# Kernel tuning notes

Hardware: AMD Instinct MI355X
Metric: run time of the kernel (lower is better)

Reference implementation:

```python
import jax, jax.numpy as jnp
import numpy as np

N = 100000      # nodes
E = 1600000     # edges (before self loops)
F_IN = 256      # num_features
HID = 8         # hid per head, layer 1
H1 = 8          # in_head
H2 = 4          # out_head
NCLS = 40       # num_classes


def setup_inputs() -> dict:
    key = jax.random.key(0)
    ks = jax.random.split(key, 10)
    p = lambda k, shape: jax.random.normal(k, shape, jnp.float32) * 0.1
    d1 = H1 * HID   # 64
    d2 = H2 * NCLS  # 160
    return dict(
        x=jax.random.normal(ks[0], (N, F_IN), jnp.float32),
        edge_index=jax.random.randint(ks[1], (2, E), 0, N),
        Wl1=p(ks[2], (F_IN, d1)), bl1=jnp.zeros((d1,), jnp.float32),
        Wr1=p(ks[3], (F_IN, d1)), br1=jnp.zeros((d1,), jnp.float32),
        att1=p(ks[4], (H1, HID)), b1=jnp.zeros((d1,), jnp.float32),
        Wl2=p(ks[5], (d1, d2)), bl2=jnp.zeros((d2,), jnp.float32),
        Wr2=p(ks[6], (d1, d2)), br2=jnp.zeros((d2,), jnp.float32),
        att2=p(ks[7], (H2, NCLS)), b2=jnp.zeros((NCLS,), jnp.float32),
    )


def gatv2_conv(x, src, dst, Wl, bl, Wr, br, att, bias, heads, ch, concat):
    """PyG GATv2Conv (eval mode): lin_l -> source/messages, lin_r -> target."""
    n = x.shape[0]
    xl = (x @ Wl + bl).reshape(n, heads, ch)   # source-side features
    xr = (x @ Wr + br).reshape(n, heads, ch)   # target-side features
    # edge-wise attention logits: LeakyReLU(x_i + x_j) . att
    e = jax.nn.leaky_relu(xl[src] + xr[dst], 0.2)          # [E, H, C]
    logits = jnp.einsum('ehc,hc->eh', e, att)               # [E, H]
    # segment softmax over incoming edges of each destination node
    m = jax.ops.segment_max(logits, dst, num_segments=n)    # [N, H]
    ex = jnp.exp(logits - m[dst])
    s = jax.ops.segment_sum(ex, dst, num_segments=n)        # [N, H]
    alpha = ex / (s[dst] + 1e-16)                           # [E, H]
    # scatter-add weighted source messages
    out = jax.ops.segment_sum(xl[src] * alpha[:, :, None], dst, num_segments=n)  # [N, H, C]
    if concat:
        return out.reshape(n, heads * ch) + bias
    return out.mean(axis=1) + bias


def reference(x, edge_index, Wl1, bl1, Wr1, br1, att1, b1,
              Wl2, bl2, Wr2, br2, att2, b2):
    n = x.shape[0]
    loop = jnp.arange(n)
    # PyG GATv2Conv default add_self_loops=True
    src = jnp.concatenate([edge_index[0], loop])
    dst = jnp.concatenate([edge_index[1], loop])
    # eval mode: all dropout (input, inter-layer, attention) disabled
    h = gatv2_conv(x, src, dst, Wl1, bl1, Wr1, br1, att1, b1, H1, HID, True)
    h = jax.nn.elu(h)
    out = gatv2_conv(h, src, dst, Wl2, bl2, Wr2, br2, att2, b2, H2, NCLS, False)
    return jax.nn.log_softmax(out, axis=1)
```

## Files before the change

kernel.cpp:

```cpp
#include <hip/hip_runtime.h>
#include <math.h>

#define NN 100000
#define EE 1600000
#define FIN 256
#define D1 64
#define D2 160
#define C2 40
#define P1R 72
#define P2R 168
#define PK1 264
#define PK2 72
#define NBUCK 391
#define CAP 5000

typedef unsigned short u16;
typedef __attribute__((ext_vector_type(8))) short bf16x8;
typedef __attribute__((ext_vector_type(4))) float f32x4;

__device__ __forceinline__ float bf2f(u16 u){ return __uint_as_float((unsigned)u << 16); }
__device__ __forceinline__ u16 f2bf(float f){
  unsigned b = __float_as_uint(f);
  return (u16)((b + 0x7FFFu + ((b >> 16) & 1u)) >> 16);
}

__global__ void wprep_k(const float* __restrict__ Wl1, const float* __restrict__ Wr1,
                        const float* __restrict__ att1,
                        const float* __restrict__ bl1, const float* __restrict__ br1,
                        const float* __restrict__ Wl2, const float* __restrict__ Wr2,
                        const float* __restrict__ att2,
                        const float* __restrict__ bl2, const float* __restrict__ br2,
                        float* __restrict__ WA1, float* __restrict__ BA1,
                        float* __restrict__ WA2, float* __restrict__ BA2){
  int t = blockIdx.x*256 + threadIdx.x;
  if (t < 4096){
    int k = t >> 4, j = t & 15;
    float v = 0.f;
    if (j < 8){
      float s = 0.f;
      #pragma unroll
      for (int c = 0; c < 8; ++c) s += Wl1[(size_t)k*D1 + j*8 + c] * att1[j*8 + c];
      v = 0.6f * s;
    }
    WA1[t] = v;
  } else if (t < 4608){
    int i = t - 4096;
    int k = i >> 3, j = i & 7;
    float v = 0.f;
    if (j < 4){
      float s = 0.f;
      #pragma unroll
      for (int c = 0; c < 40; ++c) s += Wl2[(size_t)k*D2 + j*40 + c] * att2[j*40 + c];
      v = 0.6f * s;
    }
    WA2[i] = v;
  } else if (t < 4616){
    int j = t - 4608;
    float s = 0.f;
    #pragma unroll
    for (int c = 0; c < 8; ++c) s += bl1[j*8 + c] * att1[j*8 + c];
    BA1[j] = 0.6f * s;
  } else if (t < 4620){
    int j = t - 4616;
    float s = 0.f;
    #pragma unroll
    for (int c = 0; c < 40; ++c) s += bl2[j*40 + c] * att2[j*40 + c];
    BA2[j] = 0.6f * s;
  }
}

__global__ __launch_bounds__(256) void part1_k(const int* __restrict__ ei,
                                               int* __restrict__ bcnt,
                                               int* __restrict__ csrtmp){
  __shared__ int hist[NBUCK];
  __shared__ int gbase[NBUCK];
  int t = threadIdx.x;
  for (int i = t; i < NBUCK; i += 256) hist[i] = 0;
  __syncthreads();
  int rb[8], rr[8], rv[8];
  #pragma unroll
  for (int q = 0; q < 8; ++q){
    int e = blockIdx.x*2048 + q*256 + t;
    rb[q] = -1;
    if (e < EE){
      int s = ei[e], d = ei[EE + e];
      int b = d >> 8;
      rb[q] = b;
      rv[q] = s | ((d & 255) << 17);
      rr[q] = atomicAdd(&hist[b], 1);
    }
  }
  __syncthreads();
  for (int i = t; i < NBUCK; i += 256)
    if (hist[i] > 0) gbase[i] = atomicAdd(&bcnt[i], hist[i]);
  __syncthreads();
  #pragma unroll
  for (int q = 0; q < 8; ++q){
    if (rb[q] >= 0){
      int pos = gbase[rb[q]] + rr[q];
      if (pos < CAP) csrtmp[rb[q]*CAP + pos] = rv[q];
    }
  }
}

__global__ __launch_bounds__(256) void sort_k(const int* __restrict__ bcnt,
                                              const int* __restrict__ csrtmp,
                                              int* __restrict__ csr,
                                              int* __restrict__ off,
                                              int* __restrict__ end){
  __shared__ int cnt[256];
  __shared__ int sc[256];
  __shared__ int cur[256];
  int b = blockIdx.x, t = threadIdx.x;
  int E = bcnt[b]; if (E > CAP) E = CAP;
  int n = (b << 8) + t;
  cnt[t] = (n < NN) ? 1 : 0;
  __syncthreads();
  for (int i = t; i < E; i += 256){
    int v = csrtmp[b*CAP + i];
    atomicAdd(&cnt[(v >> 17) & 255], 1);
  }
  __syncthreads();
  int x = cnt[t];
  sc[t] = x;
  __syncthreads();
  for (int o = 1; o < 256; o <<= 1){
    int v = (t >= o) ? sc[t - o] : 0;
    __syncthreads();
    sc[t] += v;
    __syncthreads();
  }
  int excl = sc[t] - x;
  if (n < NN){
    off[n] = b*CAP + excl;
    end[n] = b*CAP + excl + x;
    csr[b*CAP + excl] = n;
    cur[t] = excl + 1;
  } else {
    cur[t] = excl;
  }
  __syncthreads();
  for (int i = t; i < E; i += 256){
    int v = csrtmp[b*CAP + i];
    int p = atomicAdd(&cur[(v >> 17) & 255], 1);
    csr[b*CAP + p] = v & 0x1FFFF;
  }
}

__global__ __launch_bounds__(256) void gemm1_mfma(
    const float* __restrict__ X,
    const float* __restrict__ Wl, const float* __restrict__ bl,
    const float* __restrict__ Wr, const float* __restrict__ br,
    const float* __restrict__ WA1, const float* __restrict__ BA1,
    u16* __restrict__ outl, u16* __restrict__ outr){
  __shared__ u16 WB[144*PK1];
  int t = threadIdx.x;
  #pragma unroll
  for (int q = 0; q < 16; ++q){
    int idx = t + 256*q;
    int k = idx >> 4, c4 = idx & 15;
    float4 vl = *reinterpret_cast<const float4*>(Wl + (size_t)k*D1 + c4*4);
    float4 vr = *reinterpret_cast<const float4*>(Wr + (size_t)k*D1 + c4*4);
    WB[(c4*4+0)*PK1 + k] = f2bf(vl.x); WB[(c4*4+1)*PK1 + k] = f2bf(vl.y);
    WB[(c4*4+2)*PK1 + k] = f2bf(vl.z); WB[(c4*4+3)*PK1 + k] = f2bf(vl.w);
    WB[(64+c4*4+0)*PK1 + k] = f2bf(vr.x); WB[(64+c4*4+1)*PK1 + k] = f2bf(vr.y);
    WB[(64+c4*4+2)*PK1 + k] = f2bf(vr.z); WB[(64+c4*4+3)*PK1 + k] = f2bf(vr.w);
  }
  #pragma unroll
  for (int q = 0; q < 16; ++q){
    int idx = t + 256*q;
    int k = idx >> 4, j = idx & 15;
    WB[(128+j)*PK1 + k] = f2bf(WA1[k*16 + j]);
  }
  __syncthreads();
  int w = t >> 6, l = t & 63;
  int g = l >> 4;
  int arow = blockIdx.x*64 + w*16 + (l & 15);
  if (arow >= NN) arow = NN-1;
  const float* xp = X + (size_t)arow*FIN + g*8;
  f32x4 acc[9] = {};
  #pragma unroll
  for (int kk = 0; kk < 8; ++kk){
    float4 a0 = *reinterpret_cast<const float4*>(xp + kk*32);
    float4 a1 = *reinterpret_cast<const float4*>(xp + kk*32 + 4);
    union { bf16x8 v; u16 u[8]; } A;
    A.u[0]=f2bf(a0.x); A.u[1]=f2bf(a0.y); A.u[2]=f2bf(a0.z); A.u[3]=f2bf(a0.w);
    A.u[4]=f2bf(a1.x); A.u[5]=f2bf(a1.y); A.u[6]=f2bf(a1.z); A.u[7]=f2bf(a1.w);
    const u16* wb = WB + (l & 15)*PK1 + kk*32 + g*8;
    #pragma unroll
    for (int c = 0; c < 9; ++c){
      bf16x8 B = *reinterpret_cast<const bf16x8*>(wb + c*16*PK1);
      acc[c] = __builtin_amdgcn_mfma_f32_16x16x32_bf16(A.v, B, acc[c], 0, 0, 0);
    }
  }
  int ocol = l & 15;
  int orow0 = blockIdx.x*64 + w*16 + g*4;
  #pragma unroll
  for (int c = 0; c < 8; ++c){
    bool left = (c < 4);
    int col = (left ? c : c-4)*16 + ocol;
    u16* op = left ? outl : outr;
    float bv = (left ? bl : br)[col];
    #pragma unroll
    for (int r = 0; r < 4; ++r){
      int row = orow0 + r;
      if (row < NN) op[(size_t)row*P1R + col] = f2bf(acc[c][r] + bv);
    }
  }
  if (ocol < 8){
    float bav = BA1[ocol];
    #pragma unroll
    for (int r = 0; r < 4; ++r){
      int row = orow0 + r;
      if (row < NN) outl[(size_t)row*P1R + 64 + ocol] = f2bf(__expf(acc[8][r] + bav));
    }
  }
}

__global__ __launch_bounds__(256) void gemm2_mfma(
    const u16* __restrict__ H,
    const float* __restrict__ Wl, const float* __restrict__ bl,
    const float* __restrict__ Wr, const float* __restrict__ br,
    const float* __restrict__ WA2, const float* __restrict__ BA2,
    u16* __restrict__ outl, u16* __restrict__ outr){
  __shared__ u16 WB[336*PK2];
  int t = threadIdx.x;
  #pragma unroll
  for (int q = 0; q < 10; ++q){
    int idx = t + 256*q;
    int k = idx / 40, c4 = idx % 40;
    float4 vl = *reinterpret_cast<const float4*>(Wl + (size_t)k*D2 + c4*4);
    float4 vr = *reinterpret_cast<const float4*>(Wr + (size_t)k*D2 + c4*4);
    WB[(c4*4+0)*PK2 + k] = f2bf(vl.x); WB[(c4*4+1)*PK2 + k] = f2bf(vl.y);
    WB[(c4*4+2)*PK2 + k] = f2bf(vl.z); WB[(c4*4+3)*PK2 + k] = f2bf(vl.w);
    WB[(160+c4*4+0)*PK2 + k] = f2bf(vr.x); WB[(160+c4*4+1)*PK2 + k] = f2bf(vr.y);
    WB[(160+c4*4+2)*PK2 + k] = f2bf(vr.z); WB[(160+c4*4+3)*PK2 + k] = f2bf(vr.w);
  }
  #pragma unroll
  for (int q = 0; q < 2; ++q){
    int i2 = t + 256*q;
    int k = i2 >> 3, j = i2 & 7;
    WB[(320+j)*PK2 + k] = f2bf(WA2[k*8 + j]);
    WB[(328+j)*PK2 + k] = 0;
  }
  __syncthreads();
  int w = t >> 6, l = t & 63;
  int g = l >> 4;
  int arow = blockIdx.x*64 + w*16 + (l & 15);
  if (arow >= NN) arow = NN-1;
  const u16* hp = H + (size_t)arow*D1 + g*8;
  f32x4 acc[21] = {};
  #pragma unroll
  for (int kk = 0; kk < 2; ++kk){
    bf16x8 A = *reinterpret_cast<const bf16x8*>(hp + kk*32);
    const u16* wb = WB + (l & 15)*PK2 + kk*32 + g*8;
    #pragma unroll
    for (int c = 0; c < 21; ++c){
      bf16x8 B = *reinterpret_cast<const bf16x8*>(wb + c*16*PK2);
      acc[c] = __builtin_amdgcn_mfma_f32_16x16x32_bf16(A, B, acc[c], 0, 0, 0);
    }
  }
  int ocol = l & 15;
  int orow0 = blockIdx.x*64 + w*16 + g*4;
  #pragma unroll
  for (int c = 0; c < 20; ++c){
    bool left = (c < 10);
    int col = (left ? c : c-10)*16 + ocol;
    u16* op = left ? outl : outr;
    float bv = (left ? bl : br)[col];
    #pragma unroll
    for (int r = 0; r < 4; ++r){
      int row = orow0 + r;
      if (row < NN) op[(size_t)row*P2R + col] = f2bf(acc[c][r] + bv);
    }
  }
  if (ocol < 4){
    float bav = BA2[ocol];
    #pragma unroll
    for (int r = 0; r < 4; ++r){
      int row = orow0 + r;
      if (row < NN) outl[(size_t)row*P2R + 160 + ocol] = f2bf(__expf(acc[20][r] + bav));
    }
  }
}

__global__ void l1_fused(const u16* __restrict__ xl, const u16* __restrict__ xr,
                         const int* __restrict__ off, const int* __restrict__ end,
                         const int* __restrict__ csr,
                         const float* __restrict__ att,
                         const float* __restrict__ b, u16* __restrict__ out){
  int tid = threadIdx.x;
  int lane = tid & 63;
  int g = (lane >> 4) & 1, l = lane & 15;
  int n = blockIdx.x*8 + (tid >> 6)*2 + (lane >> 5);
  if (n >= NN) return;
  int h = l >> 1;
  ushort4 xru = *reinterpret_cast<const ushort4*>(xr + (size_t)n*P1R + 4*l);
  float xrv[4] = {bf2f(xru.x), bf2f(xru.y), bf2f(xru.z), bf2f(xru.w)};
  float a04[4];
  #pragma unroll
  for (int k = 0; k < 4; ++k) a04[k] = 0.4f * att[4*l + k];
  float s = 0.f, acc[4] = {};
  int p = off[n] + g, e1 = end[n];
  for (; p + 6 < e1; p += 8){
    int sv[4];
    #pragma unroll
    for (int q = 0; q < 4; ++q) sv[q] = csr[p + 2*q];
    ushort4 uv[4]; float wv[4];
    #pragma unroll
    for (int q = 0; q < 4; ++q){
      uv[q] = *reinterpret_cast<const ushort4*>(xl + (size_t)sv[q]*P1R + 4*l);
      wv[q] = bf2f(xl[(size_t)sv[q]*P1R + 64 + h]);
    }
    #pragma unroll
    for (int q = 0; q < 4; ++q){
      float xa[4] = {bf2f(uv[q].x), bf2f(uv[q].y), bf2f(uv[q].z), bf2f(uv[q].w)};
      float ta = 0.f;
      #pragma unroll
      for (int k = 0; k < 4; ++k) ta = fmaf(a04[k], fabsf(xa[k] + xrv[k]), ta);
      ta += __shfl_xor(ta, 1);
      float pa = __expf(ta) * wv[q];
      s += pa;
      #pragma unroll
      for (int k = 0; k < 4; ++k) acc[k] = fmaf(pa, xa[k], acc[k]);
    }
  }
  for (; p < e1; p += 2){
    int sa = csr[p];
    ushort4 ua = *reinterpret_cast<const ushort4*>(xl + (size_t)sa*P1R + 4*l);
    float wA = bf2f(xl[(size_t)sa*P1R + 64 + h]);
    float xa[4] = {bf2f(ua.x), bf2f(ua.y), bf2f(ua.z), bf2f(ua.w)};
    float ta = 0.f;
    #pragma unroll
    for (int k = 0; k < 4; ++k) ta = fmaf(a04[k], fabsf(xa[k] + xrv[k]), ta);
    ta += __shfl_xor(ta, 1);
    float pa = __expf(ta) * wA;
    s += pa;
    #pragma unroll
    for (int k = 0; k < 4; ++k) acc[k] = fmaf(pa, xa[k], acc[k]);
  }
  s += __shfl_xor(s, 16);
  #pragma unroll
  for (int k = 0; k < 4; ++k) acc[k] += __shfl_xor(acc[k], 16);
  if (g == 0){
    float inv = 1.f / (s + 1e-16f);
    ushort4 o;
    float v0 = acc[0]*inv + b[4*l+0]; o.x = f2bf(v0 > 0.f ? v0 : expm1f(v0));
    float v1 = acc[1]*inv + b[4*l+1]; o.y = f2bf(v1 > 0.f ? v1 : expm1f(v1));
    float v2 = acc[2]*inv + b[4*l+2]; o.z = f2bf(v2 > 0.f ? v2 : expm1f(v2));
    float v3 = acc[3]*inv + b[4*l+3]; o.w = f2bf(v3 > 0.f ? v3 : expm1f(v3));
    *reinterpret_cast<ushort4*>(out + (size_t)n*D1 + 4*l) = o;
  }
}

__global__ void l2_fused(const u16* __restrict__ xl, const u16* __restrict__ xr,
                         const int* __restrict__ off, const int* __restrict__ end,
                         const int* __restrict__ csr,
                         const float* __restrict__ att,
                         const float* __restrict__ b, float* __restrict__ out){
  int tid = threadIdx.x;
  int lane = tid & 63;
  int g = (lane >> 4) & 1, l = lane & 15;
  int n = blockIdx.x*8 + (tid >> 6)*2 + (lane >> 5);
  if (n >= NN) return;
  int h = l >> 2;
  int c0 = 10*l;
  float xrv[10], a04[10];
  #pragma unroll
  for (int k2 = 0; k2 < 5; ++k2){
    ushort2 u = *reinterpret_cast<const ushort2*>(xr + (size_t)n*P2R + c0 + 2*k2);
    xrv[2*k2] = bf2f(u.x); xrv[2*k2+1] = bf2f(u.y);
  }
  #pragma unroll
  for (int k = 0; k < 10; ++k) a04[k] = 0.4f * att[c0 + k];
  float s = 0.f, acc[10] = {};
  int p = off[n] + g, e1 = end[n];
  for (; p + 2 < e1; p += 4){
    int sa = csr[p], sb = csr[p+2];
    const u16* ra = xl + (size_t)sa*P2R + c0;
    const u16* rb = xl + (size_t)sb*P2R + c0;
    int dwa[5], dwb[5];
    #pragma unroll
    for (int d = 0; d < 5; ++d) dwa[d] = *reinterpret_cast<const int*>(ra + 2*d);
    #pragma unroll
    for (int d = 0; d < 5; ++d) dwb[d] = *reinterpret_cast<const int*>(rb + 2*d);
    float wA = bf2f(xl[(size_t)sa*P2R + 160 + h]);
    float wB = bf2f(xl[(size_t)sb*P2R + 160 + h]);
    float xa[10], xb[10];
    #pragma unroll
    for (int d = 0; d < 5; ++d){
      xa[2*d]   = __uint_as_float(((unsigned)dwa[d]) << 16);
      xa[2*d+1] = __uint_as_float(((unsigned)dwa[d]) & 0xFFFF0000u);
      xb[2*d]   = __uint_as_float(((unsigned)dwb[d]) << 16);
      xb[2*d+1] = __uint_as_float(((unsigned)dwb[d]) & 0xFFFF0000u);
    }
    float ta = 0.f, tb = 0.f;
    #pragma unroll
    for (int k = 0; k < 10; ++k){
      ta = fmaf(a04[k], fabsf(xa[k] + xrv[k]), ta);
      tb = fmaf(a04[k], fabsf(xb[k] + xrv[k]), tb);
    }
    ta += __shfl_xor(ta, 1); ta += __shfl_xor(ta, 2);
    tb += __shfl_xor(tb, 1); tb += __shfl_xor(tb, 2);
    float pa = __expf(ta) * wA;
    float pb = __expf(tb) * wB;
    s += pa + pb;
    #pragma unroll
    for (int k = 0; k < 10; ++k) acc[k] = fmaf(pa, xa[k], fmaf(pb, xb[k], acc[k]));
  }
  for (; p < e1; p += 2){
    int sa = csr[p];
    const u16* rp = xl + (size_t)sa*P2R + c0;
    float wA = bf2f(xl[(size_t)sa*P2R + 160 + h]);
    float xa[10];
    #pragma unroll
    for (int d = 0; d < 5; ++d){
      int u = *reinterpret_cast<const int*>(rp + 2*d);
      xa[2*d]   = __uint_as_float(((unsigned)u) << 16);
      xa[2*d+1] = __uint_as_float(((unsigned)u) & 0xFFFF0000u);
    }
    float ta = 0.f;
    #pragma unroll
    for (int k = 0; k < 10; ++k) ta = fmaf(a04[k], fabsf(xa[k] + xrv[k]), ta);
    ta += __shfl_xor(ta, 1); ta += __shfl_xor(ta, 2);
    float pa = __expf(ta) * wA;
    s += pa;
    #pragma unroll
    for (int k = 0; k < 10; ++k) acc[k] = fmaf(pa, xa[k], acc[k]);
  }
  s += __shfl_xor(s, 16);
  #pragma unroll
  for (int k = 0; k < 10; ++k) acc[k] += __shfl_xor(acc[k], 16);
  float inv = 1.f / (s + 1e-16f);
  float v[10];
  #pragma unroll
  for (int k = 0; k < 10; ++k){
    float o = acc[k] * inv;
    o += __shfl_xor(o, 4);
    o += __shfl_xor(o, 8);
    v[k] = o*0.25f + b[10*(l & 3) + k];
  }
  float mx = v[0];
  #pragma unroll
  for (int k = 1; k < 10; ++k) mx = fmaxf(mx, v[k]);
  mx = fmaxf(mx, __shfl_xor(mx, 1));
  mx = fmaxf(mx, __shfl_xor(mx, 2));
  float es = 0.f;
  #pragma unroll
  for (int k = 0; k < 10; ++k) es += __expf(v[k] - mx);
  es += __shfl_xor(es, 1);
  es += __shfl_xor(es, 2);
  float lse = mx + __logf(es);
  if (g == 0 && l < 4){
    float* op = out + (size_t)n*C2 + 10*l;
    #pragma unroll
    for (int k2 = 0; k2 < 5; ++k2)
      *reinterpret_cast<float2*>(op + 2*k2) = make_float2(v[2*k2] - lse, v[2*k2+1] - lse);
  }
}

extern "C" void kernel_launch(void* const* d_in, const int* in_sizes, int n_in,
                              void* d_out, int out_size, void* d_ws, size_t ws_size,
                              hipStream_t stream){
  const float* x    = (const float*)d_in[0];
  const int*   ei   = (const int*)  d_in[1];
  const float* Wl1  = (const float*)d_in[2];
  const float* bl1  = (const float*)d_in[3];
  const float* Wr1  = (const float*)d_in[4];
  const float* br1  = (const float*)d_in[5];
  const float* att1 = (const float*)d_in[6];
  const float* b1   = (const float*)d_in[7];
  const float* Wl2  = (const float*)d_in[8];
  const float* bl2  = (const float*)d_in[9];
  const float* Wr2  = (const float*)d_in[10];
  const float* br2  = (const float*)d_in[11];
  const float* att2 = (const float*)d_in[12];
  const float* b2   = (const float*)d_in[13];
  float* out = (float*)d_out;

  char* ws = (char*)d_ws;
  u16*   B1     = (u16*)  (ws);
  u16*   B2     = (u16*)  (ws + 15000000);
  u16*   h1     = (u16*)  (ws + 30000000);
  u16*   B3     = (u16*)  (ws + 43000000);
  u16*   B4     = (u16*)  (ws + 77000000);
  int*   csrtmp = (int*)  (ws + 77000000);
  float* WA1    = (float*)(ws + 111000000);
  float* BA1    = (float*)(ws + 111100000);
  float* WA2    = (float*)(ws + 111200000);
  float* BA2    = (float*)(ws + 111300000);
  int*   off    = (int*)  (ws + 111400000);
  int*   end    = (int*)  (ws + 111900000);
  int*   bcnt   = (int*)  (ws + 112400000);
  int*   csr    = (int*)  (ws + 112500000);
  const int blk = 256;
  const int MB = (NN + 63)/64;

  hipMemsetAsync(bcnt, 0, (size_t)NBUCK*4, stream);
  part1_k<<<(EE + 2047)/2048, blk, 0, stream>>>(ei, bcnt, csrtmp);
  sort_k <<<NBUCK, blk, 0, stream>>>(bcnt, csrtmp, csr, off, end);
  wprep_k<<<19, blk, 0, stream>>>(Wl1, Wr1, att1, bl1, br1,
                                  Wl2, Wr2, att2, bl2, br2, WA1, BA1, WA2, BA2);

  gemm1_mfma<<<MB, blk, 0, stream>>>(x, Wl1, bl1, Wr1, br1, WA1, BA1, B1, B2);
  l1_fused  <<<(NN + 7)/8, blk, 0, stream>>>(B1, B2, off, end, csr, att1, b1, h1);

  gemm2_mfma<<<MB, blk, 0, stream>>>(h1, Wl2, bl2, Wr2, br2, WA2, BA2, B3, B4);
  l2_fused  <<<(NN + 7)/8, blk, 0, stream>>>(B3, B4, off, end, csr, att2, b2, out);
}
```

Before: 353.2 us.

## Switch GAT edge features to fp16 and use packed half2 math in aggregation

The GEMM epilogues now store the node features as fp16 instead of bf16, and the per-node attention weight is scaled by 1/64. The edge loops in both layers do the LeakyReLU-dot and the weighted accumulation with packed half2 FMAs rather than per-element fp32 math. The aim is to halve the ALU instruction count in the gather-bound aggregation kernels and drop the bf16 unpacking work. The risk is reduced precision and possible overflow in the fp16 accumulators, which the 1/64 scaling partly guards against, though some accuracy is lost.

```diff
diff --git a/kernel.cpp b/kernel.cpp
--- a/kernel.cpp
+++ b/kernel.cpp
@@ -13,15 +13,23 @@
 #define PK2 72
 #define NBUCK 391
 #define CAP 5000
+#define WSCL 0.015625f
 
 typedef unsigned short u16;
 typedef __attribute__((ext_vector_type(8))) short bf16x8;
 typedef __attribute__((ext_vector_type(4))) float f32x4;
-
-__device__ __forceinline__ float bf2f(u16 u){ return __uint_as_float((unsigned)u << 16); }
+typedef _Float16 h2t __attribute__((ext_vector_type(2)));
+union hu { unsigned u; h2t h; };
+
 __device__ __forceinline__ u16 f2bf(float f){
   unsigned b = __float_as_uint(f);
   return (u16)((b + 0x7FFFu + ((b >> 16) & 1u)) >> 16);
+}
+__device__ __forceinline__ u16 f2h(float f){
+  union { _Float16 h; u16 u; } c; c.h = (_Float16)f; return c.u;
+}
+__device__ __forceinline__ float h16f(u16 v){
+  union { u16 u; _Float16 h; } c; c.u = v; return (float)c.h;
 }
 
 __global__ void wprep_k(const float* __restrict__ Wl1, const float* __restrict__ Wr1,
@@ -204,7 +212,7 @@
     #pragma unroll
     for (int r = 0; r < 4; ++r){
       int row = orow0 + r;
-      if (row < NN) op[(size_t)row*P1R + col] = f2bf(acc[c][r] + bv);
+      if (row < NN) op[(size_t)row*P1R + col] = f2h(acc[c][r] + bv);
     }
   }
   if (ocol < 8){
@@ -212,7 +220,7 @@
     #pragma unroll
     for (int r = 0; r < 4; ++r){
       int row = orow0 + r;
-      if (row < NN) outl[(size_t)row*P1R + 64 + ocol] = f2bf(__expf(acc[8][r] + bav));
+      if (row < NN) outl[(size_t)row*P1R + 64 + ocol] = f2h(__expf(acc[8][r] + bav) * WSCL);
     }
   }
 }
@@ -271,7 +279,7 @@
     #pragma unroll
     for (int r = 0; r < 4; ++r){
       int row = orow0 + r;
-      if (row < NN) op[(size_t)row*P2R + col] = f2bf(acc[c][r] + bv);
+      if (row < NN) op[(size_t)row*P2R + col] = f2h(acc[c][r] + bv);
     }
   }
   if (ocol < 4){
@@ -279,7 +287,7 @@
     #pragma unroll
     for (int r = 0; r < 4; ++r){
       int row = orow0 + r;
-      if (row < NN) outl[(size_t)row*P2R + 160 + ocol] = f2bf(__expf(acc[20][r] + bav));
+      if (row < NN) outl[(size_t)row*P2R + 160 + ocol] = f2h(__expf(acc[20][r] + bav) * WSCL);
     }
   }
 }
@@ -295,60 +303,69 @@
   int n = blockIdx.x*8 + (tid >> 6)*2 + (lane >> 5);
   if (n >= NN) return;
   int h = l >> 1;
-  ushort4 xru = *reinterpret_cast<const ushort4*>(xr + (size_t)n*P1R + 4*l);
-  float xrv[4] = {bf2f(xru.x), bf2f(xru.y), bf2f(xru.z), bf2f(xru.w)};
-  float a04[4];
-  #pragma unroll
-  for (int k = 0; k < 4; ++k) a04[k] = 0.4f * att[4*l + k];
-  float s = 0.f, acc[4] = {};
+  uint2 xru = *reinterpret_cast<const uint2*>(xr + (size_t)n*P1R + 4*l);
+  hu r0, r1; r0.u = xru.x; r1.u = xru.y;
+  hu a0, a1;
+  a0.h[0] = (_Float16)(0.4f*att[4*l+0]); a0.h[1] = (_Float16)(0.4f*att[4*l+1]);
+  a1.h[0] = (_Float16)(0.4f*att[4*l+2]); a1.h[1] = (_Float16)(0.4f*att[4*l+3]);
+  float s = 0.f;
+  hu acc0, acc1; acc0.u = 0; acc1.u = 0;
   int p = off[n] + g, e1 = end[n];
   for (; p + 6 < e1; p += 8){
     int sv[4];
     #pragma unroll
     for (int q = 0; q < 4; ++q) sv[q] = csr[p + 2*q];
-    ushort4 uv[4]; float wv[4];
+    uint2 uv[4]; u16 wv[4];
     #pragma unroll
     for (int q = 0; q < 4; ++q){
-      uv[q] = *reinterpret_cast<const ushort4*>(xl + (size_t)sv[q]*P1R + 4*l);
-      wv[q] = bf2f(xl[(size_t)sv[q]*P1R + 64 + h]);
+      uv[q] = *reinterpret_cast<const uint2*>(xl + (size_t)sv[q]*P1R + 4*l);
+      wv[q] = xl[(size_t)sv[q]*P1R + 64 + h];
     }
     #pragma unroll
     for (int q = 0; q < 4; ++q){
-      float xa[4] = {bf2f(uv[q].x), bf2f(uv[q].y), bf2f(uv[q].z), bf2f(uv[q].w)};
-      float ta = 0.f;
-      #pragma unroll
-      for (int k = 0; k < 4; ++k) ta = fmaf(a04[k], fabsf(xa[k] + xrv[k]), ta);
-      ta += __shfl_xor(ta, 1);
-      float pa = __expf(ta) * wv[q];
+      hu x0, x1; x0.u = uv[q].x; x1.u = uv[q].y;
+      hu y0, y1; y0.h = x0.h + r0.h; y1.h = x1.h + r1.h;
+      y0.u &= 0x7FFF7FFFu; y1.u &= 0x7FFF7FFFu;
+      hu t2; t2.h = a0.h*y0.h + a1.h*y1.h;
+      float tf = (float)t2.h[0] + (float)t2.h[1];
+      tf += __shfl_xor(tf, 1);
+      float pa = __expf(tf) * h16f(wv[q]);
       s += pa;
-      #pragma unroll
-      for (int k = 0; k < 4; ++k) acc[k] = fmaf(pa, xa[k], acc[k]);
+      hu pp; pp.h[0] = (_Float16)pa; pp.h[1] = pp.h[0];
+      acc0.h = pp.h*x0.h + acc0.h;
+      acc1.h = pp.h*x1.h + acc1.h;
     }
   }
   for (; p < e1; p += 2){
     int sa = csr[p];
-    ushort4 ua = *reinterpret_cast<const ushort4*>(xl + (size_t)sa*P1R + 4*l);
-    float wA = bf2f(xl[(size_t)sa*P1R + 64 + h]);
-    float xa[4] = {bf2f(ua.x), bf2f(ua.y), bf2f(ua.z), bf2f(ua.w)};
-    float ta = 0.f;
-    #pragma unroll
-    for (int k = 0; k < 4; ++k) ta = fmaf(a04[k], fabsf(xa[k] + xrv[k]), ta);
-    ta += __shfl_xor(ta, 1);
-    float pa = __expf(ta) * wA;
+    uint2 ua = *reinterpret_cast<const uint2*>(xl + (size_t)sa*P1R + 4*l);
+    u16 wa = xl[(size_t)sa*P1R + 64 + h];
+    hu x0, x1; x0.u = ua.x; x1.u = ua.y;
+    hu y0, y1; y0.h = x0.h + r0.h; y1.h = x1.h + r1.h;
+    y0.u &= 0x7FFF7FFFu; y1.u &= 0x7FFF7FFFu;
+    hu t2; t2.h = a0.h*y0.h + a1.h*y1.h;
+    float tf = (float)t2.h[0] + (float)t2.h[1];
+    tf += __shfl_xor(tf, 1);
+    float pa = __expf(tf) * h16f(wa);
     s += pa;
-    #pragma unroll
-    for (int k = 0; k < 4; ++k) acc[k] = fmaf(pa, xa[k], acc[k]);
+    hu pp; pp.h[0] = (_Float16)pa; pp.h[1] = pp.h[0];
+    acc0.h = pp.h*x0.h + acc0.h;
+    acc1.h = pp.h*x1.h + acc1.h;
   }
   s += __shfl_xor(s, 16);
-  #pragma unroll
-  for (int k = 0; k < 4; ++k) acc[k] += __shfl_xor(acc[k], 16);
+  { hu m; m.u = (unsigned)__shfl_xor((int)acc0.u, 16); acc0.h = acc0.h + m.h; }
+  { hu m; m.u = (unsigned)__shfl_xor((int)acc1.u, 16); acc1.h = acc1.h + m.h; }
   if (g == 0){
     float inv = 1.f / (s + 1e-16f);
+    float v0 = (float)acc0.h[0]*inv + b[4*l+0];
+    float v1 = (float)acc0.h[1]*inv + b[4*l+1];
+    float v2 = (float)acc1.h[0]*inv + b[4*l+2];
+    float v3 = (float)acc1.h[1]*inv + b[4*l+3];
     ushort4 o;
-    float v0 = acc[0]*inv + b[4*l+0]; o.x = f2bf(v0 > 0.f ? v0 : expm1f(v0));
-    float v1 = acc[1]*inv + b[4*l+1]; o.y = f2bf(v1 > 0.f ? v1 : expm1f(v1));
-    float v2 = acc[2]*inv + b[4*l+2]; o.z = f2bf(v2 > 0.f ? v2 : expm1f(v2));
-    float v3 = acc[3]*inv + b[4*l+3]; o.w = f2bf(v3 > 0.f ? v3 : expm1f(v3));
+    o.x = f2bf(v0 > 0.f ? v0 : expm1f(v0));
+    o.y = f2bf(v1 > 0.f ? v1 : expm1f(v1));
+    o.z = f2bf(v2 > 0.f ? v2 : expm1f(v2));
+    o.w = f2bf(v3 > 0.f ? v3 : expm1f(v3));
     *reinterpret_cast<ushort4*>(out + (size_t)n*D1 + 4*l) = o;
   }
 }
@@ -365,77 +382,91 @@
   if (n >= NN) return;
   int h = l >> 2;
   int c0 = 10*l;
-  float xrv[10], a04[10];
-  #pragma unroll
-  for (int k2 = 0; k2 < 5; ++k2){
-    ushort2 u = *reinterpret_cast<const ushort2*>(xr + (size_t)n*P2R + c0 + 2*k2);
-    xrv[2*k2] = bf2f(u.x); xrv[2*k2+1] = bf2f(u.y);
-  }
-  #pragma unroll
-  for (int k = 0; k < 10; ++k) a04[k] = 0.4f * att[c0 + k];
-  float s = 0.f, acc[10] = {};
+  hu xr2[5], a2[5];
+  #pragma unroll
+  for (int d = 0; d < 5; ++d){
+    xr2[d].u = *reinterpret_cast<const unsigned*>(xr + (size_t)n*P2R + c0 + 2*d);
+    a2[d].h[0] = (_Float16)(0.4f*att[c0 + 2*d]);
+    a2[d].h[1] = (_Float16)(0.4f*att[c0 + 2*d + 1]);
+  }
+  float s = 0.f;
+  hu acc2[5];
+  #pragma unroll
+  for (int d = 0; d < 5; ++d) acc2[d].u = 0;
   int p = off[n] + g, e1 = end[n];
   for (; p + 2 < e1; p += 4){
     int sa = csr[p], sb = csr[p+2];
     const u16* ra = xl + (size_t)sa*P2R + c0;
     const u16* rb = xl + (size_t)sb*P2R + c0;
-    int dwa[5], dwb[5];
-    #pragma unroll
-    for (int d = 0; d < 5; ++d) dwa[d] = *reinterpret_cast<const int*>(ra + 2*d);
-    #pragma unroll
-    for (int d = 0; d < 5; ++d) dwb[d] = *reinterpret_cast<const int*>(rb + 2*d);
-    float wA = bf2f(xl[(size_t)sa*P2R + 160 + h]);
-    float wB = bf2f(xl[(size_t)sb*P2R + 160 + h]);
-    float xa[10], xb[10];
+    hu xa[5], xb[5];
+    #pragma unroll
+    for (int d = 0; d < 5; ++d) xa[d].u = *reinterpret_cast<const unsigned*>(ra + 2*d);
+    #pragma unroll
+    for (int d = 0; d < 5; ++d) xb[d].u = *reinterpret_cast<const unsigned*>(rb + 2*d);
+    u16 wa16 = xl[(size_t)sa*P2R + 160 + h];
+    u16 wb16 = xl[(size_t)sb*P2R + 160 + h];
+    hu ta2, tb2; ta2.u = 0; tb2.u = 0;
     #pragma unroll
     for (int d = 0; d < 5; ++d){
-      xa[2*d]   = __uint_as_float(((unsigned)dwa[d]) << 16);
-      xa[2*d+1] = __uint_as_float(((unsigned)dwa[d]) & 0xFFFF0000u);
-      xb[2*d]   = __uint_as_float(((unsigned)dwb[d]) << 16);
-      xb[2*d+1] = __uint_as_float(((unsigned)dwb[d]) & 0xFFFF0000u);
-    }
-    float ta = 0.f, tb = 0.f;
-    #pragma unroll
-    for (int k = 0; k < 10; ++k){
-      ta = fmaf(a04[k], fabsf(xa[k] + xrv[k]), ta);
-      tb = fmaf(a04[k], fabsf(xb[k] + xrv[k]), tb);
-    }
+      hu ya, yb;
+      ya.h = xa[d].h + xr2[d].h; ya.u &= 0x7FFF7FFFu;
+      yb.h = xb[d].h + xr2[d].h; yb.u &= 0x7FFF7FFFu;
+      ta2.h = a2[d].h*ya.h + ta2.h;
+      tb2.h = a2[d].h*yb.h + tb2.h;
+    }
+    float ta = (float)ta2.h[0] + (float)ta2.h[1];
+    float tb = (float)tb2.h[0] + (float)tb2.h[1];
     ta += __shfl_xor(ta, 1); ta += __shfl_xor(ta, 2);
     tb += __shfl_xor(tb, 1); tb += __shfl_xor(tb, 2);
-    float pa = __expf(ta) * wA;
-    float pb = __expf(tb) * wB;
+    float pa = __expf(ta) * h16f(wa16);
+    float pb = __expf(tb) * h16f(wb16);
     s += pa + pb;
-    #pragma unroll
-    for (int k = 0; k < 10; ++k) acc[k] = fmaf(pa, xa[k], fmaf(pb, xb[k], acc[k]));
+    hu ppa, ppb;
+    ppa.h[0] = (_Float16)pa; ppa.h[1] = ppa.h[0];
+    ppb.h[0] = (_Float16)pb; ppb.h[1] = ppb.h[0];
+    #pragma unroll
+    for (int d = 0; d < 5; ++d){
+      acc2[d].h = ppa.h*xa[d].h + acc2[d].h;
+      acc2[d].h = ppb.h*xb[d].h + acc2[d].h;
+    }
   }
   for (; p < e1; p += 2){
     int sa = csr[p];
     const u16* rp = xl + (size_t)sa*P2R + c0;
-    float wA = bf2f(xl[(size_t)sa*P2R + 160 + h]);
-    float xa[10];
+    hu xa[5];
+    #pragma unroll
+    for (int d = 0; d < 5; ++d) xa[d].u = *reinterpret_cast<const unsigned*>(rp + 2*d);
+    u16 wa16 = xl[(size_t)sa*P2R + 160 + h];
+    hu ta2; ta2.u = 0;
     #pragma unroll
     for (int d = 0; d < 5; ++d){
-      int u = *reinterpret_cast<const int*>(rp + 2*d);
-      xa[2*d]   = __uint_as_float(((unsigned)u) << 16);
-      xa[2*d+1] = __uint_as_float(((unsigned)u) & 0xFFFF0000u);
-    }
-    float ta = 0.f;
-    #pragma unroll
-    for (int k = 0; k < 10; ++k) ta = fmaf(a04[k], fabsf(xa[k] + xrv[k]), ta);
+      hu ya; ya.h = xa[d].h + xr2[d].h; ya.u &= 0x7FFF7FFFu;
+      ta2.h = a2[d].h*ya.h + ta2.h;
+    }
+    float ta = (float)ta2.h[0] + (float)ta2.h[1];
     ta += __shfl_xor(ta, 1); ta += __shfl_xor(ta, 2);
-    float pa = __expf(ta) * wA;
+    float pa = __expf(ta) * h16f(wa16);
     s += pa;
-    #pragma unroll
-    for (int k = 0; k < 10; ++k) acc[k] = fmaf(pa, xa[k], acc[k]);
+    hu ppa; ppa.h[0] = (_Float16)pa; ppa.h[1] = ppa.h[0];
+    #pragma unroll
+    for (int d = 0; d < 5; ++d) acc2[d].h = ppa.h*xa[d].h + acc2[d].h;
   }
   s += __shfl_xor(s, 16);
   #pragma unroll
-  for (int k = 0; k < 10; ++k) acc[k] += __shfl_xor(acc[k], 16);
+  for (int d = 0; d < 5; ++d){
+    hu m; m.u = (unsigned)__shfl_xor((int)acc2[d].u, 16);
+    acc2[d].h = acc2[d].h + m.h;
+  }
   float inv = 1.f / (s + 1e-16f);
   float v[10];
   #pragma unroll
+  for (int d = 0; d < 5; ++d){
+    v[2*d]   = (float)acc2[d].h[0] * inv;
+    v[2*d+1] = (float)acc2[d].h[1] * inv;
+  }
+  #pragma unroll
   for (int k = 0; k < 10; ++k){
-    float o = acc[k] * inv;
+    float o = v[k];
     o += __shfl_xor(o, 4);
     o += __shfl_xor(o, 8);
     v[k] = o*0.25f + b[10*(l & 3) + k];
```

New measurement: 341.3 us. 1.03x faster.
